# Kernel optimization log

Hardware: AMD Instinct MI355X
Metric: run time of the kernel (lower is better)

Reference implementation:

```python
import jax, jax.numpy as jnp
import numpy as np

BATCH, D_MODEL, N_STATE, SEQ_L = 8, 1024, 64, 2048


def setup_inputs() -> dict:
    key = jax.random.key(0)
    k_u, k_a, k_b, k_c = jax.random.split(key, 4)
    scale = 1.0 / (D_MODEL * N_STATE) ** 0.5
    u = jax.random.normal(k_u, (BATCH, D_MODEL, SEQ_L), dtype=jnp.float32)
    # A is stored as a full NxN diagonal matrix, as in the torch module
    A = jnp.diag(jax.random.uniform(k_a, (N_STATE,), dtype=jnp.float32))
    B = jax.random.normal(k_b, (D_MODEL, N_STATE), dtype=jnp.float32) * scale
    C = jax.random.normal(k_c, (D_MODEL, N_STATE), dtype=jnp.float32) * scale
    return {"L": SEQ_L, "u": u, "A": A, "B": B, "C": C}


def reference(L, u, A, B, C):
    # u: (B, D, L). einsum('nn,bnd->bnd', A, h) in torch == diag(A) broadcast over h.
    a = jnp.diagonal(A)                       # (N,)
    Bu = jnp.einsum('dn,bdl->bnl', B, u)      # (B, N, L)
    Cu = jnp.einsum('dn,bdl->bnl', C, u)      # (B, N, L)
    bsz, d, _ = u.shape
    h0 = jnp.zeros((bsz, a.shape[0], d), dtype=u.dtype)  # (B, N, D)

    def step(h, xs):
        bu_l, cu_l, u_l = xs                  # (B,N), (B,N), (B,D)
        h = a[None, :, None] * h + bu_l[:, :, None] * u_l[:, None, :]
        y_l = jnp.einsum('bn,bnd->bd', cu_l, h)
        return h, y_l

    xs = (jnp.moveaxis(Bu, -1, 0), jnp.moveaxis(Cu, -1, 0), jnp.moveaxis(u, -1, 0))
    _, ys = jax.lax.scan(step, h0, xs)        # ys: (L, B, D)
    return jnp.moveaxis(ys, 0, -1)            # (B, D, L)
```

## Files before the change

kernel.cpp:

```cpp
#include <hip/hip_runtime.h>
#include <hip/hip_bf16.h>
#include <string.h>

#define BATCH 8
#define DM 1024
#define NS 64
#define SL 2048
#define NC 32
#define TC 64

typedef __attribute__((ext_vector_type(8))) short bf16x8;
typedef __attribute__((ext_vector_type(4))) float f32x4;

__device__ inline unsigned short f2bf(float f) {
    union { float f; unsigned u; } v; v.f = f;
    return (unsigned short)((v.u + 0x7fffu + ((v.u >> 16) & 1u)) >> 16);
}
__device__ inline float bf2f(unsigned short h) {
    return __uint_as_float(((unsigned)h) << 16);
}


__global__ __launch_bounds__(256) void k_prep(const float* __restrict__ Bm,
                                              const float* __restrict__ Cm,
                                              unsigned short* __restrict__ BT,
                                              unsigned short* __restrict__ CT)
{
    __shared__ float sT[64][65];
    const float* src = blockIdx.y ? Cm : Bm;
    unsigned short* dst = blockIdx.y ? CT : BT;
    const int d0 = blockIdx.x * 64, t = threadIdx.x;
    {
        int r = t >> 2, f = (t & 3) * 16;
#pragma unroll
        for (int i = 0; i < 4; i++) {
            float4 v = *(const float4*)&src[(size_t)(d0 + r) * NS + f + i * 4];
            sT[r][f + i * 4 + 0] = v.x; sT[r][f + i * 4 + 1] = v.y;
            sT[r][f + i * 4 + 2] = v.z; sT[r][f + i * 4 + 3] = v.w;
        }
    }
    __syncthreads();
    {
        int n = t >> 2, dq = (t & 3) * 16;
        unsigned pk[8];
#pragma unroll
        for (int k = 0; k < 8; k++) {
            unsigned short a = f2bf(sT[dq + 2 * k][n]);
            unsigned short bb = f2bf(sT[dq + 2 * k + 1][n]);
            pk[k] = (unsigned)a | ((unsigned)bb << 16);
        }
        uint4 v0 = { pk[0], pk[1], pk[2], pk[3] };
        uint4 v1 = { pk[4], pk[5], pk[6], pk[7] };
        *(uint4*)&dst[(size_t)n * DM + d0 + dq] = v0;
        *(uint4*)&dst[(size_t)n * DM + d0 + dq + 8] = v1;
    }
}

__global__ __launch_bounds__(512) void k_proj(const float* __restrict__ u,
                                              const unsigned short* __restrict__ BC,
                                              unsigned short* __restrict__ BuT,
                                              unsigned short* __restrict__ CuT,
                                              unsigned short* __restrict__ Ubf)
{
    __shared__ unsigned short sA[32 * 64];
    __shared__ unsigned short sB[128 * 64];
    const int b = blockIdx.y, l0 = blockIdx.x * 32, t = threadIdx.x;
    const int lane = t & 63, w = t >> 6, g = lane >> 4, m15 = lane & 15;
    const int dd = t >> 3, c8 = t & 7;
    const int dq = dd >> 3, d7 = dd & 7;

    f32x4 acc[2];
    acc[0] = (f32x4){0.f, 0.f, 0.f, 0.f};
    acc[1] = (f32x4){0.f, 0.f, 0.f, 0.f};

#pragma unroll 1
    for (int d0 = 0; d0 < DM; d0 += 64) {
        __syncthreads();
        {
            float4 v = *(const float4*)&u[((size_t)b * DM + d0 + dd) * SL + l0 + c8 * 4];
            unsigned short b0 = f2bf(v.x), b1 = f2bf(v.y), b2 = f2bf(v.z), b3 = f2bf(v.w);
            int l = c8 * 4;
            sA[(l + 0) * 64 + ((dq ^ ((l + 0) & 7)) * 8) + d7] = b0;
            sA[(l + 1) * 64 + ((dq ^ ((l + 1) & 7)) * 8) + d7] = b1;
            sA[(l + 2) * 64 + ((dq ^ ((l + 2) & 7)) * 8) + d7] = b2;
            sA[(l + 3) * 64 + ((dq ^ ((l + 3) & 7)) * 8) + d7] = b3;
            uint2 pk = { (unsigned)b0 | ((unsigned)b1 << 16),
                         (unsigned)b2 | ((unsigned)b3 << 16) };
            *(uint2*)(Ubf + ((size_t)b * DM + d0 + dd) * SL + l0 + c8 * 4) = pk;
        }
#pragma unroll
        for (int p = 0; p < 2; p++) {
            int idx = p * 512 + t;
            int row = idx >> 3, cc8 = idx & 7;
            uint4 v = *(const uint4*)(BC + (size_t)row * DM + d0 + cc8 * 8);
            *(uint4*)&sB[row * 64 + ((cc8 ^ (row & 7)) * 8)] = v;
        }
        __syncthreads();
#pragma unroll
        for (int ks = 0; ks < 2; ks++) {
            bf16x8 af[2], bfr;
#pragma unroll
            for (int mt = 0; mt < 2; mt++) {
                int r = mt * 16 + m15;
                af[mt] = *(const bf16x8*)&sA[r * 64 + (((ks * 4 + g) ^ (r & 7)) * 8)];
            }
            {
                int r = w * 16 + m15;
                bfr = *(const bf16x8*)&sB[r * 64 + (((ks * 4 + g) ^ (r & 7)) * 8)];
            }
#pragma unroll
            for (int mt = 0; mt < 2; mt++)
                acc[mt] = __builtin_amdgcn_mfma_f32_16x16x32_bf16(af[mt], bfr, acc[mt], 0, 0, 0);
        }
    }
    {
        int wn = w * 16 + m15;
        unsigned short* dst = (wn < 64) ? BuT : CuT;
        int n = wn & 63;
#pragma unroll
        for (int mt = 0; mt < 2; mt++)
#pragma unroll
            for (int r = 0; r < 4; r++) {
                int l = l0 + mt * 16 + g * 4 + r;
                dst[((size_t)b * SL + l) * NS + n] = f2bf(acc[mt][r]);
            }
    }
}

__global__ __launch_bounds__(256) void k_g(const float* __restrict__ A,
                                           const unsigned short* __restrict__ BuT,
                                           const unsigned short* __restrict__ CuT,
                                           unsigned short* __restrict__ Gw,
                                           unsigned short* __restrict__ Bvw,
                                           unsigned short* __restrict__ Wcw)
{
    __shared__ unsigned short sCu[64 * 64];
    __shared__ unsigned short sBu[8 * 64 * 8];
    __shared__ unsigned short sP[8 * 66 * 8];
    __shared__ unsigned short sTb[64 * 66];
    const int cc = blockIdx.x, b = cc >> 5, c = cc & 31;
    const int gy = blockIdx.y;
    const int t = threadIdx.x, lane = t & 63;
    const int l0 = c * TC;
    const size_t gbase = (size_t)cc * 4096;

    {
        const unsigned short* srcC = CuT + ((size_t)b * SL + l0) * NS;
        const unsigned short* srcB = BuT + ((size_t)b * SL + l0) * NS;
#pragma unroll
        for (int p = 0; p < 2; p++) {
            int idx = p * 256 + t;
            int r = idx >> 3, q8 = idx & 7;
            uint4 vc = *(const uint4*)(srcC + (size_t)r * NS + q8 * 8);
            *(uint4*)&sCu[r * 64 + q8 * 8] = vc;
            uint4 vb = *(const uint4*)(srcB + (size_t)r * NS + q8 * 8);
            *(uint4*)&sBu[(q8 * 64 + r) * 8] = vb;
        }
    }
    {
        int n = t & 63;
        float an = A[n * NS + n];
        int q = n >> 3, n7 = n & 7;
#pragma unroll 1
        for (int dl = (t >> 6) * 17; dl < (t >> 6) * 17 + 17 && dl <= 64; dl++)
            sP[(q * 66 + dl) * 8 + n7] = f2bf(__powf(an, (float)dl));
    }
    __syncthreads();

#pragma unroll 1
    for (int r = gy * 8; r < gy * 8 + 8; r++) {
        int idx = r * 256 + t;
        int l = idx >> 6;
        int lp = lane;
        int dl = l - lp;
        float acc = 0.f;
        if (dl >= 0) {
#pragma unroll
            for (int q = 0; q < 8; q++) {
                bf16x8 cu = *(const bf16x8*)&sCu[l * 64 + q * 8];
                bf16x8 bu = *(const bf16x8*)&sBu[(q * 64 + lp) * 8];
                bf16x8 pp = *(const bf16x8*)&sP[(q * 66 + dl) * 8];
#pragma unroll
                for (int j = 0; j < 8; j++)
                    acc = fmaf(bf2f((unsigned short)cu[j]) * bf2f((unsigned short)bu[j]),
                               bf2f((unsigned short)pp[j]), acc);
            }
        }
        Gw[gbase + l * 64 + lp] = (dl >= 0) ? f2bf(acc) : (unsigned short)0;
    }

    if (gy == 0) {
#pragma unroll 1
        for (int r = 0; r < 16; r++) {
            int idx = r * 256 + t;
            int l = idx >> 6;
            int n = lane, q = n >> 3, n7 = n & 7;
            float cu = bf2f(sCu[l * 64 + n]);
            float pv = bf2f(sP[(q * 66 + (l + 1)) * 8 + n7]);
            Wcw[gbase + l * 64 + n] = f2bf(cu * pv);
        }
    } else {
#pragma unroll 1
        for (int r = 0; r < 16; r++) {
            int idx = r * 256 + t;
            int l = idx >> 6;
            int n = lane, q = n >> 3, n7 = n & 7;
            float bu = bf2f(sBu[(q * 64 + l) * 8 + n7]);
            float pv = bf2f(sP[(q * 66 + (63 - l)) * 8 + n7]);
            sTb[n * 66 + l] = f2bf(bu * pv);
        }
        __syncthreads();
#pragma unroll 1
        for (int r = 0; r < 16; r++) {
            int idx = r * 256 + t;
            int n = idx >> 6;
            int l = lane;
            Bvw[gbase + n * 64 + l] = sTb[n * 66 + l];
        }
    }
}

__global__ __launch_bounds__(256) void k_scan2(const unsigned short* __restrict__ Ubf,
                                               const unsigned short* __restrict__ Gw,
                                               const unsigned short* __restrict__ Bvw,
                                               const unsigned short* __restrict__ Wcw,
                                               const float* __restrict__ A,
                                               float* __restrict__ y)
{
    __shared__ unsigned short sU[32 * 64];
    __shared__ unsigned short sG[64 * 64];
    __shared__ unsigned short sV[64 * 64];
    __shared__ unsigned short sW[64 * 64];
    __shared__ unsigned short sH[32 * 64];
    const int slab = blockIdx.x, b = blockIdx.y;
    const int d0 = slab * 32;
    const int t = threadIdx.x, lane = t & 63, w = t >> 6, g = lane >> 4, m15 = lane & 15;
    const int rr = t >> 3, c8 = t & 7;

    const int n_own = w * 16 + m15;
    const float pw = __powf(A[n_own * NS + n_own], (float)TC);

    *(uint4*)&sH[t * 8] = (uint4){0u, 0u, 0u, 0u};
    float hsf[8];
#pragma unroll
    for (int i = 0; i < 8; i++) hsf[i] = 0.f;

    const unsigned short* ub = Ubf + ((size_t)b * DM + d0 + rr) * SL + c8 * 8;
    const size_t gb0 = ((size_t)b * NC) * 4096;

    uint4 pU, pG[2], pV[2], pW[2];
    pU = *(const uint4*)(ub);
#pragma unroll
    for (int p = 0; p < 2; p++) {
        size_t ro = (size_t)(p * 32 + rr) * 64 + c8 * 8;
        pG[p] = *(const uint4*)(Gw + gb0 + ro);
        pV[p] = *(const uint4*)(Bvw + gb0 + ro);
        pW[p] = *(const uint4*)(Wcw + gb0 + ro);
    }

#pragma unroll 1
    for (int c = 0; c < NC; c++) {
        *(uint4*)&sU[rr * 64 + ((c8 ^ (rr & 7)) * 8)] = pU;
#pragma unroll
        for (int p = 0; p < 2; p++) {
            int row = p * 32 + rr;
            *(uint4*)&sG[row * 64 + ((c8 ^ (row & 7)) * 8)] = pG[p];
            *(uint4*)&sV[row * 64 + ((c8 ^ (row & 7)) * 8)] = pV[p];
            *(uint4*)&sW[row * 64 + ((c8 ^ (row & 7)) * 8)] = pW[p];
        }
        __syncthreads();

        if (c + 1 < NC) {
            pU = *(const uint4*)(ub + (c + 1) * 64);
            size_t gb = gb0 + (size_t)(c + 1) * 4096;
#pragma unroll
            for (int p = 0; p < 2; p++) {
                size_t ro = (size_t)(p * 32 + rr) * 64 + c8 * 8;
                pG[p] = *(const uint4*)(Gw + gb + ro);
                pV[p] = *(const uint4*)(Bvw + gb + ro);
                pW[p] = *(const uint4*)(Wcw + gb + ro);
            }
        }

        f32x4 accY[2], accE[2];
        accY[0] = (f32x4){0.f, 0.f, 0.f, 0.f}; accY[1] = accY[0];
        accE[0] = accY[0]; accE[1] = accY[0];

#pragma unroll
        for (int ks = 0; ks < 2; ks++) {
            int kq = ks * 4 + g;
            int r0 = m15, r1 = 16 + m15;
            int rg = w * 16 + m15;
            bf16x8 af0 = *(const bf16x8*)&sU[r0 * 64 + ((kq ^ (r0 & 7)) * 8)];
            bf16x8 af1 = *(const bf16x8*)&sU[r1 * 64 + ((kq ^ (r1 & 7)) * 8)];
            bf16x8 ah0 = *(const bf16x8*)&sH[r0 * 64 + ((kq ^ (r0 & 7)) * 8)];
            bf16x8 ah1 = *(const bf16x8*)&sH[r1 * 64 + ((kq ^ (r1 & 7)) * 8)];
            bf16x8 bg  = *(const bf16x8*)&sG[rg * 64 + ((kq ^ (rg & 7)) * 8)];
            bf16x8 bw_ = *(const bf16x8*)&sW[rg * 64 + ((kq ^ (rg & 7)) * 8)];
            bf16x8 bv  = *(const bf16x8*)&sV[rg * 64 + ((kq ^ (rg & 7)) * 8)];
            accY[0] = __builtin_amdgcn_mfma_f32_16x16x32_bf16(af0, bg,  accY[0], 0, 0, 0);
            accY[1] = __builtin_amdgcn_mfma_f32_16x16x32_bf16(af1, bg,  accY[1], 0, 0, 0);
            accY[0] = __builtin_amdgcn_mfma_f32_16x16x32_bf16(ah0, bw_, accY[0], 0, 0, 0);
            accY[1] = __builtin_amdgcn_mfma_f32_16x16x32_bf16(ah1, bw_, accY[1], 0, 0, 0);
            accE[0] = __builtin_amdgcn_mfma_f32_16x16x32_bf16(af0, bv,  accE[0], 0, 0, 0);
            accE[1] = __builtin_amdgcn_mfma_f32_16x16x32_bf16(af1, bv,  accE[1], 0, 0, 0);
        }

        {
            float* yb = y + ((size_t)b * DM + d0 + g * 4) * SL + c * 64 + w * 16 + m15;
#pragma unroll
            for (int mt = 0; mt < 2; mt++)
#pragma unroll
                for (int r = 0; r < 4; r++)
                    yb[(size_t)(mt * 16 + r) * SL] = accY[mt][r];
        }

#pragma unroll
        for (int mt = 0; mt < 2; mt++)
#pragma unroll
            for (int r = 0; r < 4; r++)
                hsf[mt * 4 + r] = fmaf(pw, hsf[mt * 4 + r], accE[mt][r]);

        __syncthreads();

        if (c + 1 < NC) {
            int nq = n_own >> 3, n7 = n_own & 7;
#pragma unroll
            for (int mt = 0; mt < 2; mt++)
#pragma unroll
                for (int r = 0; r < 4; r++) {
                    int dd = mt * 16 + g * 4 + r;
                    sH[dd * 64 + ((nq ^ (dd & 7)) * 8) + n7] = f2bf(hsf[mt * 4 + r]);
                }
        }
    }
}

extern "C" void kernel_launch(void* const* d_in, const int* in_sizes, int n_in,
                              void* d_out, int out_size, void* d_ws, size_t ws_size,
                              hipStream_t stream) {
    const float* u = (const float*)d_in[1];
    const float* A = (const float*)d_in[2];
    const float* B = (const float*)d_in[3];
    const float* C = (const float*)d_in[4];
    float* y = (float*)d_out;

    char* base = (char*)d_ws;
    unsigned short* BuT = (unsigned short*)(base);
    unsigned short* CuT = (unsigned short*)(base + (2u << 20));
    unsigned short* BT  = (unsigned short*)(base + (4u << 20));
    unsigned short* Gw  = (unsigned short*)(base + (5u << 20));
    unsigned short* Bvw = (unsigned short*)(base + (7u << 20));
    unsigned short* Wcw = (unsigned short*)(base + (9u << 20));
    unsigned short* Ubf = (unsigned short*)(base + (44u << 20));
    unsigned short* CT  = BT + (size_t)NS * DM;

    k_prep<<<dim3(DM / 64, 2), 256, 0, stream>>>(B, C, BT, CT);
    k_proj<<<dim3(SL / 32, BATCH), 512, 0, stream>>>(u, BT, BuT, CuT, Ubf);
    k_g<<<dim3(BATCH * NC, 2), 256, 0, stream>>>(A, BuT, CuT, Gw, Bvw, Wcw);
    k_scan2<<<dim3(DM / 32, BATCH), 256, 0, stream>>>(Ubf, Gw, Bvw, Wcw, A, y);
}
```

Before: 119.0 us.

## Split sequential chunk scan into grouped state pass, prefix scan, and output pass

Replaces the single sequential 32-chunk scan kernel with three kernels. First, 8 chunk groups each compute their local end state in parallel. Then a small kernel prefix-scans those group states. Finally, each group computes its outputs from the carried-in state. This multiplies grid parallelism by 8, from 256 blocks to 2048, to shorten the serial critical path. The cost is two extra launches, a second pass over U and Bv, and bf16 rounding of the intermediate group states.

```diff
diff --git a/kernel.cpp b/kernel.cpp
--- a/kernel.cpp
+++ b/kernel.cpp
@@ -8,9 +8,12 @@
 #define SL 2048
 #define NC 32
 #define TC 64
+#define NG 8
+#define CG 4
 
 typedef __attribute__((ext_vector_type(8))) short bf16x8;
 typedef __attribute__((ext_vector_type(4))) float f32x4;
+typedef float v2f __attribute__((ext_vector_type(2)));
 
 __device__ inline unsigned short f2bf(float f) {
     union { float f; unsigned u; } v; v.f = f;
@@ -18,6 +21,10 @@
 }
 __device__ inline float bf2f(unsigned short h) {
     return __uint_as_float(((unsigned)h) << 16);
+}
+static __device__ inline v2f bfpair_to_v2f(unsigned int p) {
+    unsigned int lo = p << 16, hi = p & 0xffff0000u;
+    v2f r; r.x = __uint_as_float(lo); r.y = __uint_as_float(hi); return r;
 }
 
 
@@ -220,33 +227,144 @@
     }
 }
 
-__global__ __launch_bounds__(256) void k_scan2(const unsigned short* __restrict__ Ubf,
-                                               const unsigned short* __restrict__ Gw,
-                                               const unsigned short* __restrict__ Bvw,
-                                               const unsigned short* __restrict__ Wcw,
-                                               const float* __restrict__ A,
-                                               float* __restrict__ y)
+__global__ __launch_bounds__(256) void k_stateg(const unsigned short* __restrict__ Ubf,
+                                                const unsigned short* __restrict__ Bvw,
+                                                const float* __restrict__ A,
+                                                unsigned short* __restrict__ Eg)
+{
+    __shared__ unsigned short sU[32 * 64];
+    __shared__ unsigned short sV[64 * 64];
+    const int slab = blockIdx.x, b = blockIdx.y, gg = blockIdx.z;
+    const int d0 = slab * 32;
+    const int t = threadIdx.x, lane = t & 63, w = t >> 6, g = lane >> 4, m15 = lane & 15;
+    const int rr = t >> 3, c8 = t & 7;
+
+    const int n_own = w * 16 + m15;
+    const float pw = __powf(A[n_own * NS + n_own], (float)TC);
+
+    float hsf[8];
+#pragma unroll
+    for (int i = 0; i < 8; i++) hsf[i] = 0.f;
+
+    const unsigned short* ub = Ubf + ((size_t)b * DM + d0 + rr) * SL + gg * CG * 64 + c8 * 8;
+    const size_t gb0 = ((size_t)(b * NC + gg * CG)) * 4096;
+
+    uint4 pU, pV[2];
+    pU = *(const uint4*)(ub);
+#pragma unroll
+    for (int p = 0; p < 2; p++)
+        pV[p] = *(const uint4*)(Bvw + gb0 + (size_t)(p * 32 + rr) * 64 + c8 * 8);
+
+#pragma unroll 1
+    for (int c = 0; c < CG; c++) {
+        *(uint4*)&sU[rr * 64 + ((c8 ^ (rr & 7)) * 8)] = pU;
+#pragma unroll
+        for (int p = 0; p < 2; p++) {
+            int row = p * 32 + rr;
+            *(uint4*)&sV[row * 64 + ((c8 ^ (row & 7)) * 8)] = pV[p];
+        }
+        __syncthreads();
+
+        if (c + 1 < CG) {
+            pU = *(const uint4*)(ub + (c + 1) * 64);
+            size_t gb = gb0 + (size_t)(c + 1) * 4096;
+#pragma unroll
+            for (int p = 0; p < 2; p++)
+                pV[p] = *(const uint4*)(Bvw + gb + (size_t)(p * 32 + rr) * 64 + c8 * 8);
+        }
+
+        f32x4 accE[2];
+        accE[0] = (f32x4){0.f, 0.f, 0.f, 0.f};
+        accE[1] = accE[0];
+#pragma unroll
+        for (int ks = 0; ks < 2; ks++) {
+            int kq = ks * 4 + g;
+            int r0 = m15, r1 = 16 + m15, rg = w * 16 + m15;
+            bf16x8 af0 = *(const bf16x8*)&sU[r0 * 64 + ((kq ^ (r0 & 7)) * 8)];
+            bf16x8 af1 = *(const bf16x8*)&sU[r1 * 64 + ((kq ^ (r1 & 7)) * 8)];
+            bf16x8 bv  = *(const bf16x8*)&sV[rg * 64 + ((kq ^ (rg & 7)) * 8)];
+            accE[0] = __builtin_amdgcn_mfma_f32_16x16x32_bf16(af0, bv, accE[0], 0, 0, 0);
+            accE[1] = __builtin_amdgcn_mfma_f32_16x16x32_bf16(af1, bv, accE[1], 0, 0, 0);
+        }
+#pragma unroll
+        for (int mt = 0; mt < 2; mt++)
+#pragma unroll
+            for (int r = 0; r < 4; r++)
+                hsf[mt * 4 + r] = fmaf(pw, hsf[mt * 4 + r], accE[mt][r]);
+
+        __syncthreads();
+    }
+#pragma unroll
+    for (int mt = 0; mt < 2; mt++)
+#pragma unroll
+        for (int r = 0; r < 4; r++) {
+            int dd = d0 + mt * 16 + g * 4 + r;
+            Eg[((size_t)(b * NG + gg) * DM + dd) * NS + n_own] = f2bf(hsf[mt * 4 + r]);
+        }
+}
+
+__global__ __launch_bounds__(256) void k_prefixg(const float* __restrict__ A,
+                                                 unsigned short* __restrict__ Eg)
+{
+    int gg = blockIdx.x * 256 + threadIdx.x;
+    int p  = gg & 31;
+    int d  = (gg >> 5) & (DM - 1);
+    int b  = gg >> 15;
+    int n0 = p * 2;
+
+    float a0 = A[n0 * NS + n0];
+    float a1 = A[(n0 + 1) * NS + (n0 + 1)];
+    v2f aT = { __powf(a0, (float)(TC * CG)), __powf(a1, (float)(TC * CG)) };
+    v2f hs = { 0.f, 0.f };
+
+    unsigned int* base = (unsigned int*)Eg + ((((size_t)b * NG) * DM + d) * NS >> 1) + p;
+    const size_t cstride = ((size_t)DM * NS) >> 1;
+
+#pragma unroll
+    for (int c = 0; c < NG; c++) {
+        unsigned int* ptr = base + (size_t)c * cstride;
+        unsigned int e = *ptr;
+        unsigned int sw = (unsigned)f2bf(hs.x) | ((unsigned)f2bf(hs.y) << 16);
+        *ptr = sw;
+        hs = __builtin_elementwise_fma(aT, hs, bfpair_to_v2f(e));
+    }
+}
+
+__global__ __launch_bounds__(256) void k_yg(const unsigned short* __restrict__ Ubf,
+                                            const unsigned short* __restrict__ Gw,
+                                            const unsigned short* __restrict__ Bvw,
+                                            const unsigned short* __restrict__ Wcw,
+                                            const unsigned short* __restrict__ HSg,
+                                            const float* __restrict__ A,
+                                            float* __restrict__ y)
 {
     __shared__ unsigned short sU[32 * 64];
     __shared__ unsigned short sG[64 * 64];
     __shared__ unsigned short sV[64 * 64];
     __shared__ unsigned short sW[64 * 64];
     __shared__ unsigned short sH[32 * 64];
-    const int slab = blockIdx.x, b = blockIdx.y;
+    const int slab = blockIdx.x, b = blockIdx.y, gg = blockIdx.z;
     const int d0 = slab * 32;
     const int t = threadIdx.x, lane = t & 63, w = t >> 6, g = lane >> 4, m15 = lane & 15;
     const int rr = t >> 3, c8 = t & 7;
 
     const int n_own = w * 16 + m15;
+    const int nq = n_own >> 3, n7 = n_own & 7;
     const float pw = __powf(A[n_own * NS + n_own], (float)TC);
 
-    *(uint4*)&sH[t * 8] = (uint4){0u, 0u, 0u, 0u};
     float hsf[8];
 #pragma unroll
-    for (int i = 0; i < 8; i++) hsf[i] = 0.f;
-
-    const unsigned short* ub = Ubf + ((size_t)b * DM + d0 + rr) * SL + c8 * 8;
-    const size_t gb0 = ((size_t)b * NC) * 4096;
+    for (int mt = 0; mt < 2; mt++)
+#pragma unroll
+        for (int r = 0; r < 4; r++) {
+            int dd = mt * 16 + g * 4 + r;
+            unsigned short hv = HSg[((size_t)(b * NG + gg) * DM + d0 + dd) * NS + n_own];
+            hsf[mt * 4 + r] = bf2f(hv);
+            sH[dd * 64 + ((nq ^ (dd & 7)) * 8) + n7] = hv;
+        }
+
+    const unsigned short* ub = Ubf + ((size_t)b * DM + d0 + rr) * SL + gg * CG * 64 + c8 * 8;
+    const size_t gb0 = ((size_t)(b * NC + gg * CG)) * 4096;
 
     uint4 pU, pG[2], pV[2], pW[2];
     pU = *(const uint4*)(ub);
@@ -259,7 +377,7 @@
     }
 
 #pragma unroll 1
-    for (int c = 0; c < NC; c++) {
+    for (int c = 0; c < CG; c++) {
         *(uint4*)&sU[rr * 64 + ((c8 ^ (rr & 7)) * 8)] = pU;
 #pragma unroll
         for (int p = 0; p < 2; p++) {
@@ -270,7 +388,7 @@
         }
         __syncthreads();
 
-        if (c + 1 < NC) {
+        if (c + 1 < CG) {
             pU = *(const uint4*)(ub + (c + 1) * 64);
             size_t gb = gb0 + (size_t)(c + 1) * 4096;
 #pragma unroll
@@ -289,8 +407,7 @@
 #pragma unroll
         for (int ks = 0; ks < 2; ks++) {
             int kq = ks * 4 + g;
-            int r0 = m15, r1 = 16 + m15;
-            int rg = w * 16 + m15;
+            int r0 = m15, r1 = 16 + m15, rg = w * 16 + m15;
             bf16x8 af0 = *(const bf16x8*)&sU[r0 * 64 + ((kq ^ (r0 & 7)) * 8)];
             bf16x8 af1 = *(const bf16x8*)&sU[r1 * 64 + ((kq ^ (r1 & 7)) * 8)];
             bf16x8 ah0 = *(const bf16x8*)&sH[r0 * 64 + ((kq ^ (r0 & 7)) * 8)];
@@ -307,7 +424,7 @@
         }
 
         {
-            float* yb = y + ((size_t)b * DM + d0 + g * 4) * SL + c * 64 + w * 16 + m15;
+            float* yb = y + ((size_t)b * DM + d0 + g * 4) * SL + (gg * CG + c) * 64 + w * 16 + m15;
 #pragma unroll
             for (int mt = 0; mt < 2; mt++)
 #pragma unroll
@@ -323,8 +440,7 @@
 
         __syncthreads();
 
-        if (c + 1 < NC) {
-            int nq = n_own >> 3, n7 = n_own & 7;
+        if (c + 1 < CG) {
 #pragma unroll
             for (int mt = 0; mt < 2; mt++)
 #pragma unroll
@@ -352,11 +468,14 @@
     unsigned short* Gw  = (unsigned short*)(base + (5u << 20));
     unsigned short* Bvw = (unsigned short*)(base + (7u << 20));
     unsigned short* Wcw = (unsigned short*)(base + (9u << 20));
+    unsigned short* Eg  = (unsigned short*)(base + (11u << 20));
     unsigned short* Ubf = (unsigned short*)(base + (44u << 20));
     unsigned short* CT  = BT + (size_t)NS * DM;
 
     k_prep<<<dim3(DM / 64, 2), 256, 0, stream>>>(B, C, BT, CT);
     k_proj<<<dim3(SL / 32, BATCH), 512, 0, stream>>>(u, BT, BuT, CuT, Ubf);
     k_g<<<dim3(BATCH * NC, 2), 256, 0, stream>>>(A, BuT, CuT, Gw, Bvw, Wcw);
-    k_scan2<<<dim3(DM / 32, BATCH), 256, 0, stream>>>(Ubf, Gw, Bvw, Wcw, A, y);
-}
+    k_stateg<<<dim3(DM / 32, BATCH, NG), 256, 0, stream>>>(Ubf, Bvw, A, Eg);
+    k_prefixg<<<dim3(BATCH * DM * 32 / 256), 256, 0, stream>>>(A, Eg);
+    k_yg<<<dim3(DM / 32, BATCH, NG), 256, 0, stream>>>(Ubf, Gw, Bvw, Wcw, Eg, A, y);
+}
```

New measurement: 145.2 us. +22.0%, slower.
